# Kernel tuning notes

Measured on AMD Instinct MI355X. Metric: run time of the kernel, lower is better.

The kernel has to match this reference:

```python
import jax, jax.numpy as jnp
import numpy as np

B, D_IN, D_HID, E, K = 524288, 256, 512, 16, 2


def setup_inputs() -> dict:
    key = jax.random.key(0)
    kx, k1, kb1, k2, kb2 = jax.random.split(key, 5)
    s1 = 1.0 / np.sqrt(D_IN)
    s2 = 1.0 / np.sqrt(D_HID)
    return {
        "x": jax.random.normal(kx, (B, D_IN), dtype=jnp.float32),
        "w1": jax.random.uniform(k1, (D_IN, D_HID), jnp.float32, -s1, s1),
        "b1": jax.random.uniform(kb1, (D_HID,), jnp.float32, -s1, s1),
        "w2": jax.random.uniform(k2, (D_HID, E), jnp.float32, -s2, s2),
        "b2": jax.random.uniform(kb2, (E,), jnp.float32, -s2, s2),
    }


def reference(x, w1, b1, w2, b2):
    # 2-layer MLP router
    h = jax.nn.relu(x @ w1 + b1)            # [B, D_HID]
    logits = h @ w2 + b2                    # [B, E]
    # top-k mask (1.0 at top-k expert slots, 0.0 elsewhere)
    _, topk_idx = jax.lax.top_k(logits, K)  # [B, K]
    mask = jax.nn.one_hot(topk_idx, E, dtype=logits.dtype).sum(axis=-2)  # [B, E]
    # NOTE: faithful to original — non-topk logits are zeroed (not -inf),
    # then softmax is taken over ALL experts including the zeros.
    sparse_logits = logits * mask
    weights = jax.nn.softmax(sparse_logits, axis=-1)
    return weights
```

## Files before the change

kernel.cpp:

```cpp
#include <hip/hip_runtime.h>
#include <cmath>

#define NE   16
#define DIN  256
#define DHID 512
#define NROW 524288
#define ROWS 64
#define TAU  4e-4f

typedef __bf16 bf16;
typedef bf16  bf16x8 __attribute__((ext_vector_type(8)));
typedef float f32x4  __attribute__((ext_vector_type(4)));

template<int CTRL>
__device__ __forceinline__ float dpp_xor_add(float v) {
    int s = __builtin_amdgcn_update_dpp(0, __float_as_int(v), CTRL, 0xF, 0xF, true);
    return v + __int_as_float(s);
}
template<int OFF>
__device__ __forceinline__ float swz_xor_add(float v) {
    int s = __builtin_amdgcn_ds_swizzle(__float_as_int(v), OFF);
    return v + __int_as_float(s);
}
__device__ __forceinline__ void load_lds16(const void* g, void* l) {
    __builtin_amdgcn_global_load_lds(
        (const __attribute__((address_space(1))) void*)g,
        (__attribute__((address_space(3))) void*)l,
        16, 0, 0);
}

__global__ __launch_bounds__(256)
void split_w1_k(const float* __restrict__ w1, bf16* __restrict__ w1t) {
    int i = blockIdx.x * 256 + threadIdx.x;
    int col = i & 511, k = i >> 9;
    float v = w1[k * DHID + col];
    bf16 h = (bf16)v;
    bf16 l = (bf16)(v - (float)h);
    int ch = col >> 7, cl = col & 127, ksk = k >> 5, g = (k >> 3) & 3, j = k & 7;
    size_t base = (size_t)(ch * 8 + ksk) * 8192;
    w1t[base +        g * 1024 + cl * 8 + j] = h;
    w1t[base + 4096 + g * 1024 + cl * 8 + j] = l;
}

__global__ __launch_bounds__(256, 2)
void router_mfma_k(const float* __restrict__ x,
                   const float* __restrict__ b1,
                   const float* __restrict__ w2,
                   const float* __restrict__ b2,
                   float* __restrict__ out,
                   const bf16* __restrict__ w1t,
                   unsigned* __restrict__ cnt,
                   unsigned* __restrict__ ids,
                   unsigned cap)
{
    __shared__ __align__(16) bf16 xh_s[8][4][ROWS][8];
    __shared__ __align__(16) bf16 xl_s[8][4][ROWS][8];
    __shared__ __align__(16) bf16 w_s[2][4][128][8];
    float* l_lds = (float*)&w_s[0][0][0][0];

    const int t    = threadIdx.x;
    const int lane = t & 63;
    const int wv   = t >> 6;
    const int wr   = wv >> 1;
    const int wc   = wv & 1;
    const int c    = lane & 15;
    const int g    = lane >> 4;
    const long long row0 = (long long)blockIdx.x * ROWS;

    {
        const int r = t & 63;
        const float* xg = x + (row0 + r) * DIN + wv * 64;
#pragma unroll
        for (int m = 0; m < 8; ++m) {
            float4 v0 = ((const float4*)xg)[2 * m];
            float4 v1 = ((const float4*)xg)[2 * m + 1];
            int k   = wv * 64 + m * 8;
            int ksk = k >> 5, gg = (k >> 3) & 3;
            float vv[8] = {v0.x, v0.y, v0.z, v0.w, v1.x, v1.y, v1.z, v1.w};
            bf16 hb[8], lb[8];
#pragma unroll
            for (int q = 0; q < 8; ++q) {
                hb[q] = (bf16)vv[q];
                lb[q] = (bf16)(vv[q] - (float)hb[q]);
            }
            *(bf16x8*)&xh_s[ksk][gg][r][0] = *(const bf16x8*)hb;
            *(bf16x8*)&xl_s[ksk][gg][r][0] = *(const bf16x8*)lb;
        }
    }

    float lg[8];
#pragma unroll
    for (int i = 0; i < 8; ++i) lg[i] = 0.f;

    for (int ch = 0; ch < 4; ++ch) {
        f32x4 acc[2][4];
#pragma unroll
        for (int ti = 0; ti < 2; ++ti)
#pragma unroll
            for (int tj = 0; tj < 4; ++tj)
#pragma unroll
                for (int r = 0; r < 4; ++r) acc[ti][tj][r] = 0.f;

        for (int ksk = 0; ksk < 8; ++ksk) {
            __syncthreads();
            {
                const bf16* src = w1t + (size_t)(ch * 8 + ksk) * 8192
                                      + wv * 2048 + lane * 8;
                bf16* dst = ((bf16*)w_s) + wv * 2048;
#pragma unroll
                for (int p = 0; p < 4; ++p)
                    load_lds16(src + p * 512, dst + p * 512);
            }
            __syncthreads();

            bf16x8 ah[2], al[2];
#pragma unroll
            for (int ti = 0; ti < 2; ++ti) {
                ah[ti] = *(const bf16x8*)&xh_s[ksk][g][32 * wr + 16 * ti + c][0];
                al[ti] = *(const bf16x8*)&xl_s[ksk][g][32 * wr + 16 * ti + c][0];
            }
#pragma unroll
            for (int tj = 0; tj < 4; ++tj) {
                bf16x8 bh = *(const bf16x8*)&w_s[0][g][64 * wc + 16 * tj + c][0];
                bf16x8 bl = *(const bf16x8*)&w_s[1][g][64 * wc + 16 * tj + c][0];
#pragma unroll
                for (int ti = 0; ti < 2; ++ti) {
                    acc[ti][tj] = __builtin_amdgcn_mfma_f32_16x16x32_bf16(ah[ti], bh, acc[ti][tj], 0, 0, 0);
                    acc[ti][tj] = __builtin_amdgcn_mfma_f32_16x16x32_bf16(ah[ti], bl, acc[ti][tj], 0, 0, 0);
                    acc[ti][tj] = __builtin_amdgcn_mfma_f32_16x16x32_bf16(al[ti], bh, acc[ti][tj], 0, 0, 0);
                }
            }
        }

#pragma unroll
        for (int tj = 0; tj < 4; ++tj) {
            float bj = b1[128 * ch + 64 * wc + 16 * tj + c];
#pragma unroll
            for (int ti = 0; ti < 2; ++ti)
#pragma unroll
                for (int r = 0; r < 4; ++r)
                    acc[ti][tj][r] = fmaxf(acc[ti][tj][r] + bj, 0.f);
        }

#pragma unroll 1
        for (int e = 0; e < NE; ++e) {
            float p[8];
#pragma unroll
            for (int i = 0; i < 8; ++i) p[i] = 0.f;
#pragma unroll
            for (int tj = 0; tj < 4; ++tj) {
                float wvv = w2[(128 * ch + 64 * wc + 16 * tj + c) * NE + e];
#pragma unroll
                for (int ti = 0; ti < 2; ++ti)
#pragma unroll
                    for (int r = 0; r < 4; ++r)
                        p[ti * 4 + r] = fmaf(acc[ti][tj][r], wvv, p[ti * 4 + r]);
            }
#pragma unroll
            for (int i = 0; i < 8; ++i) p[i] = dpp_xor_add<0xB1>(p[i]);
#pragma unroll
            for (int i = 0; i < 8; ++i) p[i] = dpp_xor_add<0x4E>(p[i]);
#pragma unroll
            for (int i = 0; i < 8; ++i) p[i] = swz_xor_add<0x101F>(p[i]);
#pragma unroll
            for (int i = 0; i < 8; ++i) p[i] = swz_xor_add<0x201F>(p[i]);
            if (c == e) {
#pragma unroll
                for (int i = 0; i < 8; ++i) lg[i] += p[i];
            }
        }
    }

    __syncthreads();
    if (wc == 0) {
        float b2c = b2[c];
#pragma unroll
        for (int ti = 0; ti < 2; ++ti)
#pragma unroll
            for (int r = 0; r < 4; ++r)
                l_lds[(32 * wr + 16 * ti + 4 * g + r) * (NE + 1) + c] = lg[ti * 4 + r] + b2c;
    }
    __syncthreads();
    if (wc == 1) {
#pragma unroll
        for (int ti = 0; ti < 2; ++ti)
#pragma unroll
            for (int r = 0; r < 4; ++r)
                l_lds[(32 * wr + 16 * ti + 4 * g + r) * (NE + 1) + c] += lg[ti * 4 + r];
    }
    __syncthreads();

    if (t < ROWS) {
        float l[NE];
#pragma unroll
        for (int e = 0; e < NE; ++e) l[e] = l_lds[t * (NE + 1) + e];

        float m1 = -INFINITY; int i1 = 0;
#pragma unroll
        for (int e = 0; e < NE; ++e)
            if (l[e] > m1) { m1 = l[e]; i1 = e; }
        float m2 = -INFINITY; int i2 = -1;
#pragma unroll
        for (int e = 0; e < NE; ++e)
            if (e != i1 && l[e] > m2) { m2 = l[e]; i2 = e; }
        float m3 = -INFINITY;
#pragma unroll
        for (int e = 0; e < NE; ++e)
            if (e != i1 && e != i2 && l[e] > m3) m3 = l[e];

        if (m2 - m3 < TAU) {
            unsigned idx = atomicAdd(cnt, 1u);
            if (idx < cap) ids[idx] = (unsigned)(row0 + t);
        }

        float s[NE];
#pragma unroll
        for (int e = 0; e < NE; ++e)
            s[e] = (e == i1 || e == i2) ? l[e] : 0.f;
        float mx = s[0];
#pragma unroll
        for (int e = 1; e < NE; ++e) mx = fmaxf(mx, s[e]);
        float ex[NE];
        float sum = 0.f;
#pragma unroll
        for (int e = 0; e < NE; ++e) { ex[e] = expf(s[e] - mx); sum += ex[e]; }
        float r = 1.f / sum;
        float4 o0 = {ex[0] * r, ex[1] * r, ex[2] * r, ex[3] * r};
        float4 o1 = {ex[4] * r, ex[5] * r, ex[6] * r, ex[7] * r};
        float4 o2 = {ex[8] * r, ex[9] * r, ex[10] * r, ex[11] * r};
        float4 o3 = {ex[12] * r, ex[13] * r, ex[14] * r, ex[15] * r};
        float4* og = (float4*)(out + (row0 + t) * NE);
        og[0] = o0; og[1] = o1; og[2] = o2; og[3] = o3;
    }
}

__global__ __launch_bounds__(256)
void fixup_k(const float* __restrict__ x,
             const float* __restrict__ w1,
             const float* __restrict__ b1,
             const float* __restrict__ w2,
             const float* __restrict__ b2,
             float* __restrict__ out,
             const unsigned* __restrict__ cntp,
             const unsigned* __restrict__ ids,
             unsigned cap)
{
    const int lane = threadIdx.x & 63;
    const int gw   = (int)((blockIdx.x * 256 + threadIdx.x) >> 6);
    const int nw   = (int)((gridDim.x * 256) >> 6);
    unsigned n = *cntp; if (n > cap) n = cap;
    const int c = lane & 15;
    const int g = lane >> 4;

    for (unsigned wi = gw; wi < n; wi += nw) {
        unsigned row = ids[wi];
        const float* xr = x + (size_t)row * DIN;
        const int nh0 = 128 * g;
        int cols[8];
#pragma unroll
        for (int j = 0; j < 8; ++j)
            cols[j] = nh0 + c * 4 + (j & 3) + ((j >> 2) << 6);

        float a[8];
#pragma unroll
        for (int j = 0; j < 8; ++j) a[j] = 0.f;
        for (int k4 = 0; k4 < 64; ++k4) {
            float4 xv = *(const float4*)(xr + k4 * 4);
            const float* wp = w1 + (size_t)(k4 * 4) * DHID;
#pragma unroll
            for (int j = 0; j < 8; ++j) {
                a[j] = fmaf(xv.x, wp[cols[j]],            a[j]);
                a[j] = fmaf(xv.y, wp[DHID + cols[j]],     a[j]);
                a[j] = fmaf(xv.z, wp[2 * DHID + cols[j]], a[j]);
                a[j] = fmaf(xv.w, wp[3 * DHID + cols[j]], a[j]);
            }
        }
        float h[8];
#pragma unroll
        for (int j = 0; j < 8; ++j) h[j] = fmaxf(a[j] + b1[cols[j]], 0.f);

        float l[NE];
#pragma unroll 1
        for (int e = 0; e < NE; ++e) {
            float p = 0.f;
#pragma unroll
            for (int j = 0; j < 8; ++j)
                p = fmaf(h[j], w2[cols[j] * NE + e], p);
            p += __shfl_xor(p, 1, 64);
            p += __shfl_xor(p, 2, 64);
            p += __shfl_xor(p, 4, 64);
            p += __shfl_xor(p, 8, 64);
            float t0 = __shfl(p, 0 * 16 + e, 64);
            float t1 = __shfl(p, 1 * 16 + e, 64);
            float t2 = __shfl(p, 2 * 16 + e, 64);
            float t3 = __shfl(p, 3 * 16 + e, 64);
            l[e] = (((t0 + t1) + t2) + t3) + b2[e];
        }

        if (lane == 0) {
            float m1 = -INFINITY; int i1 = 0;
#pragma unroll
            for (int e = 0; e < NE; ++e)
                if (l[e] > m1) { m1 = l[e]; i1 = e; }
            float m2 = -INFINITY; int i2 = -1;
#pragma unroll
            for (int e = 0; e < NE; ++e)
                if (e != i1 && l[e] > m2) { m2 = l[e]; i2 = e; }
            float s[NE];
#pragma unroll
            for (int e = 0; e < NE; ++e)
                s[e] = (e == i1 || e == i2) ? l[e] : 0.f;
            float mx = s[0];
#pragma unroll
            for (int e = 1; e < NE; ++e) mx = fmaxf(mx, s[e]);
            float ex[NE];
            float sum = 0.f;
#pragma unroll
            for (int e = 0; e < NE; ++e) { ex[e] = expf(s[e] - mx); sum += ex[e]; }
            float* og = out + (size_t)row * NE;
#pragma unroll
            for (int e = 0; e < NE; ++e) og[e] = ex[e] / sum;
        }
    }
}

extern "C" void kernel_launch(void* const* d_in, const int* in_sizes, int n_in,
                              void* d_out, int out_size, void* d_ws, size_t ws_size,
                              hipStream_t stream) {
    const float* x  = (const float*)d_in[0];
    const float* w1 = (const float*)d_in[1];
    const float* b1 = (const float*)d_in[2];
    const float* w2 = (const float*)d_in[3];
    const float* b2 = (const float*)d_in[4];
    float* outp = (float*)d_out;

    bf16*     w1t = (bf16*)d_ws;
    unsigned* cnt = (unsigned*)((char*)d_ws + (1u << 20));
    unsigned* ids = (unsigned*)((char*)d_ws + (1u << 20) + 64);
    unsigned  cap = 0;
    if (ws_size > (1u << 20) + 64)
        cap = (unsigned)((ws_size - (1u << 20) - 64) / 4);

    hipMemsetAsync((char*)d_ws + (1u << 20), 0, 4, stream);
    split_w1_k<<<dim3(512), dim3(256), 0, stream>>>(w1, w1t);
    router_mfma_k<<<dim3(NROW / ROWS), dim3(256), 0, stream>>>(
        x, b1, w2, b2, outp, w1t, cnt, ids, cap);
    fixup_k<<<dim3(256), dim3(256), 0, stream>>>(
        x, w1, b1, w2, b2, outp, cnt, ids, cap);
}
```

Before: 1.399 ms.

## Load W1 fragments directly to registers with double-buffered prefetch, drop LDS staging

W1 tiles are no longer staged through shared memory with two barriers per k-step. Each wave now reads its bf16 hi/lo W1 fragments straight from global memory (L2-resident) into registers. The loop is software-pipelined with A/B register buffers, so the next step's W and X fragments load while the current MFMAs run. This removes most block-level syncs and LDS traffic, but adds register pressure and redundant global reads of W1 across waves.

```diff
diff --git a/kernel.cpp b/kernel.cpp
--- a/kernel.cpp
+++ b/kernel.cpp
@@ -21,12 +21,6 @@
 __device__ __forceinline__ float swz_xor_add(float v) {
     int s = __builtin_amdgcn_ds_swizzle(__float_as_int(v), OFF);
     return v + __int_as_float(s);
-}
-__device__ __forceinline__ void load_lds16(const void* g, void* l) {
-    __builtin_amdgcn_global_load_lds(
-        (const __attribute__((address_space(1))) void*)g,
-        (__attribute__((address_space(3))) void*)l,
-        16, 0, 0);
 }
 
 __global__ __launch_bounds__(256)
@@ -41,6 +35,37 @@
     w1t[base +        g * 1024 + cl * 8 + j] = h;
     w1t[base + 4096 + g * 1024 + cl * 8 + j] = l;
 }
+
+#define LOADW(W, si)                                                              \
+    {                                                                             \
+        const bf16* sp = w1t + (size_t)(si) * 8192 + g * 1024 + (64 * wc + c) * 8;\
+        _Pragma("unroll")                                                         \
+        for (int tj = 0; tj < 4; ++tj) {                                          \
+            W[tj][0] = *(const bf16x8*)(sp + tj * 128);                           \
+            W[tj][1] = *(const bf16x8*)(sp + tj * 128 + 4096);                    \
+        }                                                                         \
+    }
+
+#define LOADX(X, kk)                                                              \
+    {                                                                             \
+        _Pragma("unroll")                                                         \
+        for (int ti = 0; ti < 2; ++ti) {                                          \
+            X[ti][0] = *(const bf16x8*)&xh_s[kk][g][32 * wr + 16 * ti + c][0];    \
+            X[ti][1] = *(const bf16x8*)&xl_s[kk][g][32 * wr + 16 * ti + c][0];    \
+        }                                                                         \
+    }
+
+#define COMPUTE(X, W)                                                             \
+    {                                                                             \
+        _Pragma("unroll")                                                         \
+        for (int tj = 0; tj < 4; ++tj)                                            \
+            _Pragma("unroll")                                                     \
+            for (int ti = 0; ti < 2; ++ti) {                                      \
+                acc[ti][tj] = __builtin_amdgcn_mfma_f32_16x16x32_bf16(X[ti][0], W[tj][0], acc[ti][tj], 0, 0, 0); \
+                acc[ti][tj] = __builtin_amdgcn_mfma_f32_16x16x32_bf16(X[ti][0], W[tj][1], acc[ti][tj], 0, 0, 0); \
+                acc[ti][tj] = __builtin_amdgcn_mfma_f32_16x16x32_bf16(X[ti][1], W[tj][0], acc[ti][tj], 0, 0, 0); \
+            }                                                                     \
+    }
 
 __global__ __launch_bounds__(256, 2)
 void router_mfma_k(const float* __restrict__ x,
@@ -55,8 +80,7 @@
 {
     __shared__ __align__(16) bf16 xh_s[8][4][ROWS][8];
     __shared__ __align__(16) bf16 xl_s[8][4][ROWS][8];
-    __shared__ __align__(16) bf16 w_s[2][4][128][8];
-    float* l_lds = (float*)&w_s[0][0][0][0];
+    __shared__ float l_lds[ROWS][NE + 1];
 
     const int t    = threadIdx.x;
     const int lane = t & 63;
@@ -69,28 +93,34 @@
 
     {
         const int r = t & 63;
-        const float* xg = x + (row0 + r) * DIN + wv * 64;
+        const int q = t >> 6;
+        const float* xg = x + (row0 + r) * DIN + q * 64;
 #pragma unroll
         for (int m = 0; m < 8; ++m) {
             float4 v0 = ((const float4*)xg)[2 * m];
             float4 v1 = ((const float4*)xg)[2 * m + 1];
-            int k   = wv * 64 + m * 8;
+            int k   = q * 64 + m * 8;
             int ksk = k >> 5, gg = (k >> 3) & 3;
             float vv[8] = {v0.x, v0.y, v0.z, v0.w, v1.x, v1.y, v1.z, v1.w};
             bf16 hb[8], lb[8];
 #pragma unroll
-            for (int q = 0; q < 8; ++q) {
-                hb[q] = (bf16)vv[q];
-                lb[q] = (bf16)(vv[q] - (float)hb[q]);
+            for (int qq = 0; qq < 8; ++qq) {
+                hb[qq] = (bf16)vv[qq];
+                lb[qq] = (bf16)(vv[qq] - (float)hb[qq]);
             }
             *(bf16x8*)&xh_s[ksk][gg][r][0] = *(const bf16x8*)hb;
             *(bf16x8*)&xl_s[ksk][gg][r][0] = *(const bf16x8*)lb;
         }
     }
+    __syncthreads();
 
     float lg[8];
 #pragma unroll
     for (int i = 0; i < 8; ++i) lg[i] = 0.f;
+
+    bf16x8 wA[4][2], wB[4][2], xA[2][2], xB[2][2];
+    LOADW(wA, 0);
+    LOADX(xA, 0);
 
     for (int ch = 0; ch < 4; ++ch) {
         f32x4 acc[2][4];
@@ -101,35 +131,17 @@
 #pragma unroll
                 for (int r = 0; r < 4; ++r) acc[ti][tj][r] = 0.f;
 
-        for (int ksk = 0; ksk < 8; ++ksk) {
-            __syncthreads();
-            {
-                const bf16* src = w1t + (size_t)(ch * 8 + ksk) * 8192
-                                      + wv * 2048 + lane * 8;
-                bf16* dst = ((bf16*)w_s) + wv * 2048;
-#pragma unroll
-                for (int p = 0; p < 4; ++p)
-                    load_lds16(src + p * 512, dst + p * 512);
-            }
-            __syncthreads();
-
-            bf16x8 ah[2], al[2];
-#pragma unroll
-            for (int ti = 0; ti < 2; ++ti) {
-                ah[ti] = *(const bf16x8*)&xh_s[ksk][g][32 * wr + 16 * ti + c][0];
-                al[ti] = *(const bf16x8*)&xl_s[ksk][g][32 * wr + 16 * ti + c][0];
-            }
-#pragma unroll
-            for (int tj = 0; tj < 4; ++tj) {
-                bf16x8 bh = *(const bf16x8*)&w_s[0][g][64 * wc + 16 * tj + c][0];
-                bf16x8 bl = *(const bf16x8*)&w_s[1][g][64 * wc + 16 * tj + c][0];
-#pragma unroll
-                for (int ti = 0; ti < 2; ++ti) {
-                    acc[ti][tj] = __builtin_amdgcn_mfma_f32_16x16x32_bf16(ah[ti], bh, acc[ti][tj], 0, 0, 0);
-                    acc[ti][tj] = __builtin_amdgcn_mfma_f32_16x16x32_bf16(ah[ti], bl, acc[ti][tj], 0, 0, 0);
-                    acc[ti][tj] = __builtin_amdgcn_mfma_f32_16x16x32_bf16(al[ti], bh, acc[ti][tj], 0, 0, 0);
-                }
-            }
+#pragma unroll
+        for (int kp = 0; kp < 4; ++kp) {
+            const int ks0 = 2 * kp;
+            int s1 = ch * 8 + ks0 + 1; if (s1 > 31) s1 = 31;
+            int s2 = ch * 8 + ks0 + 2; if (s2 > 31) s2 = 31;
+            LOADW(wB, s1);
+            LOADX(xB, (ks0 + 1) & 7);
+            COMPUTE(xA, wA);
+            LOADW(wA, s2);
+            LOADX(xA, (ks0 + 2) & 7);
+            COMPUTE(xB, wB);
         }
 
 #pragma unroll
@@ -178,7 +190,7 @@
         for (int ti = 0; ti < 2; ++ti)
 #pragma unroll
             for (int r = 0; r < 4; ++r)
-                l_lds[(32 * wr + 16 * ti + 4 * g + r) * (NE + 1) + c] = lg[ti * 4 + r] + b2c;
+                l_lds[32 * wr + 16 * ti + 4 * g + r][c] = lg[ti * 4 + r] + b2c;
     }
     __syncthreads();
     if (wc == 1) {
@@ -186,14 +198,14 @@
         for (int ti = 0; ti < 2; ++ti)
 #pragma unroll
             for (int r = 0; r < 4; ++r)
-                l_lds[(32 * wr + 16 * ti + 4 * g + r) * (NE + 1) + c] += lg[ti * 4 + r];
+                l_lds[32 * wr + 16 * ti + 4 * g + r][c] += lg[ti * 4 + r];
     }
     __syncthreads();
 
     if (t < ROWS) {
         float l[NE];
 #pragma unroll
-        for (int e = 0; e < NE; ++e) l[e] = l_lds[t * (NE + 1) + e];
+        for (int e = 0; e < NE; ++e) l[e] = l_lds[t][e];
 
         float m1 = -INFINITY; int i1 = 0;
 #pragma unroll
```

Result: faster. 1.370 ms (-2.1%).
